# Performance work log

Hardware: AMD Instinct MI355X
Metric: run time of the kernel (lower is better)

## Reference

```python
import jax, jax.numpy as jnp
import numpy as np

B, DIMX, DIMY, DIMH = 256, 128, 128, 128
SMOOTH, CONVEX = 2.0, 1.0
MAX_IT, TOL = 500, 1e-3
sp = jax.nn.softplus


def setup_inputs() -> dict:
    key = jax.random.key(0)
    ks = jax.random.split(key, 32)
    def p(k, *shape):
        # xavier-ish small init for weights/biases
        return (jax.random.normal(k, shape, dtype=jnp.float32) * 0.05)
    return {
        'x': jax.random.normal(ks[0], (B, DIMX), dtype=jnp.float32),
        'y': jax.random.normal(ks[1], (B, DIMY), dtype=jnp.float32),
        # first block (Wuus[0], Wyus[0], Wys[0], Wus[0])
        'wuu0_w': p(ks[2], DIMH, DIMX), 'wuu0_b': p(ks[3], DIMH),
        'wyu0_w': p(ks[4], DIMY, DIMX), 'wyu0_b': p(ks[5], DIMY),
        'wy0': p(ks[6], DIMH, DIMY),
        'wu0_w': p(ks[7], DIMH, DIMX), 'wu0_b': p(ks[8], DIMH),
        # middle block (Wuus[1], Wzus[0], Wzs[0], Wyus[1], Wys[1], Wus[1])
        'wuu1_w': p(ks[9], DIMH, DIMH), 'wuu1_b': p(ks[10], DIMH),
        'wzu1_w': p(ks[11], DIMH, DIMH), 'wzu1_b': p(ks[12], DIMH),
        'wz1': p(ks[13], DIMH, DIMH),
        'wyu1_w': p(ks[14], DIMY, DIMH), 'wyu1_b': p(ks[15], DIMY),
        'wy1': p(ks[16], DIMH, DIMY),
        'wu1_w': p(ks[17], DIMH, DIMH), 'wu1_b': p(ks[18], DIMH),
        # last block (Wzus[-1], Wzs[-1], Wyus[-1], Wys[-1], Wus[-1])
        'wzu2_w': p(ks[19], 1, DIMH), 'wzu2_b': p(ks[20], 1),
        'wz2': p(ks[21], 1, DIMH),
        'wyu2_w': p(ks[22], DIMY, DIMH), 'wyu2_b': p(ks[23], DIMY),
        'wy2': p(ks[24], 1, DIMY),
        'wu2_w': p(ks[25], 1, DIMH), 'wu2_b': p(ks[26], 1),
    }


def reference(x, y, wuu0_w, wuu0_b, wyu0_w, wyu0_b, wy0, wu0_w, wu0_b,
              wuu1_w, wuu1_b, wzu1_w, wzu1_b, wz1, wyu1_w, wyu1_b, wy1, wu1_w, wu1_b,
              wzu2_w, wzu2_b, wz2, wyu2_w, wyu2_b, wy2, wu2_w, wu2_b):
    # ICNN scalar output summed over batch (per-sample outputs decouple in y)
    def icnn_sum(y_):
        u0 = sp(x @ wuu0_w.T + wuu0_b)                                   # [B,H]
        z = sp((y_ * (x @ wyu0_w.T + wyu0_b)) @ wy0.T + x @ wu0_w.T + wu0_b)
        u1 = sp(u0 @ wuu1_w.T + wuu1_b)
        zu = sp(u0 @ wzu1_w.T + wzu1_b)
        z = sp((z * zu) @ jnp.clip(wz1, 0.0, 1e10).T
               + (y_ * (u0 @ wyu1_w.T + wyu1_b)) @ wy1.T
               + u0 @ wu1_w.T + wu1_b)
        zu2 = sp(u1 @ wzu2_w.T + wzu2_b)                                 # [B,1]
        z = ((z * zu2) @ jnp.clip(wz2, 0.0, 1e10).T
             + (y_ * (u1 @ wyu2_w.T + wyu2_b)) @ wy2.T
             + u1 @ wu2_w.T + wu2_b)                                     # [B,1]
        out = z + (0.5 / SMOOTH) * jnp.sum(y_ * y_, axis=1, keepdims=True)
        return jnp.sum(out)

    grad_icnn = jax.grad(icnn_sum)
    step = 2.0 * SMOOTH

    def body(carry, i):
        y1, done = carry
        g = grad_icnn(y1)
        y1_new = y1 + (step / (i + 1.0)) * (y - g)
        conv = jnp.mean(jnp.linalg.norm(y - g, axis=1)) < TOL
        y1 = jnp.where(done, y1, y1_new)  # freeze after 'break'
        return (y1, done | conv), None

    y1_init = jnp.ones_like(y)
    (y1, _), _ = jax.lax.scan(body, (y1_init, jnp.asarray(False)),
                              jnp.arange(MAX_IT, dtype=jnp.float32))
    f_ast1 = y1 + CONVEX * y
    return jnp.mean(f_ast1, axis=1).reshape(-1, 1)
```

## Files before the change

### kernel.cpp

```cpp
#include <hip/hip_runtime.h>
#include <math.h>

#define NB 256
#define N 128
#define NTHREADS 512
#define MAX_IT 500
#define ALF0 0.41256f
#define ALF1 1.73581f
#define ALF2 0.53115f
#define ALF3 0.89502f
#define SLICE 40
#define SLOT(k) ((((k) >> 5) * SLICE) + ((k) & 31))
#define LDSVEC (3 * SLICE + 32)


template <int CTRL>
__device__ __forceinline__ float dpp_add(float p) {
    return p + __int_as_float(__builtin_amdgcn_update_dpp(
                   0, __float_as_int(p), CTRL, 0xF, 0xF, true));
}
__device__ __forceinline__ float quad_sum(float p) {
    p = dpp_add<0xB1>(p);
    p = dpp_add<0x4E>(p);
    return p;
}
__device__ __forceinline__ float row_sum16(float p) {
    p = quad_sum(p);
    p = dpp_add<0x124>(p);
    p = dpp_add<0x128>(p);
    return p;
}
__device__ __forceinline__ float wave_sum(float p) {
    p += __shfl_xor(p, 1);
    p += __shfl_xor(p, 2);
    p += __shfl_xor(p, 4);
    p += __shfl_xor(p, 8);
    p += __shfl_xor(p, 16);
    p += __shfl_xor(p, 32);
    return p;
}
__device__ __forceinline__ float softplus_f(float s) {
    float e = __expf(-fabsf(s));
    return fmaxf(s, 0.f) + __logf(1.f + e);
}
__device__ __forceinline__ float sigmoid_f(float s) {
    float e = __expf(-fabsf(s));
    float r = 1.f / (1.f + e);
    return s >= 0.f ? r : 1.f - r;
}

__device__ __forceinline__ float mv_row(const float* __restrict__ W,
                                        const float* __restrict__ V,
                                        int k, int h) {
    const float4* wr = (const float4*)(W + k * N + h * 32);
    const float4* vr = (const float4*)(V + h * SLICE);
    float q0 = 0.f, q1 = 0.f, q2 = 0.f, q3 = 0.f;
#pragma unroll
    for (int i = 0; i < 8; ++i) {
        float4 w = wr[i], v = vr[i];
        q0 = fmaf(w.x, v.x, q0); q1 = fmaf(w.y, v.y, q1);
        q2 = fmaf(w.z, v.z, q2); q3 = fmaf(w.w, v.w, q3);
    }
    return quad_sum((q0 + q1) + (q2 + q3));
}

__global__ __launch_bounds__(NTHREADS, 2)
void picnn_solve(const float* __restrict__ x, const float* __restrict__ y,
                 const float* __restrict__ wuu0_w, const float* __restrict__ wuu0_b,
                 const float* __restrict__ wyu0_w, const float* __restrict__ wyu0_b,
                 const float* __restrict__ wy0,
                 const float* __restrict__ wu0_w, const float* __restrict__ wu0_b,
                 const float* __restrict__ wuu1_w, const float* __restrict__ wuu1_b,
                 const float* __restrict__ wzu1_w, const float* __restrict__ wzu1_b,
                 const float* __restrict__ wz1,
                 const float* __restrict__ wyu1_w, const float* __restrict__ wyu1_b,
                 const float* __restrict__ wy1,
                 const float* __restrict__ wu1_w, const float* __restrict__ wu1_b,
                 const float* __restrict__ wzu2_w, const float* __restrict__ wzu2_b,
                 const float* __restrict__ wz2,
                 const float* __restrict__ wyu2_w, const float* __restrict__ wyu2_b,
                 const float* __restrict__ wy2,
                 float* __restrict__ out)
{
    const int b = blockIdx.x;
    const int t = threadIdx.x;
    const int k = t >> 2;
    const int h = t & 3;
    const int wave = t >> 6;
    const int lane = t & 63;

    __shared__ __align__(16) float xv[LDSVEC];
    __shared__ __align__(16) float u0v[LDSVEC];
    __shared__ __align__(16) float u1v[LDSVEC];
    __shared__ __align__(16) float a0s[LDSVEC];
    __shared__ __align__(16) float a1s[LDSVEC];
    __shared__ __align__(16) float y1s[LDSVEC];
    __shared__ __align__(16) float t1s[LDSVEC];
    __shared__ __align__(16) float d2s[LDSVEC];
    __shared__ __align__(16) float d1s[LDSVEC];
    __shared__ float rp[8];
    __shared__ __align__(16) float4 img1[8 * NTHREADS];
    __shared__ __align__(16) float4 img2[8 * NTHREADS];

    if (t < N) xv[SLOT(t)] = x[b * N + t];
    __syncthreads();

    float u0k = softplus_f(mv_row(wuu0_w, xv, k, h) + wuu0_b[k]);
    float a0k = mv_row(wyu0_w, xv, k, h) + wyu0_b[k];
    float c0  = mv_row(wu0_w,  xv, k, h) + wu0_b[k];
    if (h == 0) { u0v[SLOT(k)] = u0k; a0s[SLOT(k)] = a0k; }
    __syncthreads();

    float u1k = softplus_f(mv_row(wuu1_w, u0v, k, h) + wuu1_b[k]);
    float zu  = softplus_f(mv_row(wzu1_w, u0v, k, h) + wzu1_b[k]);
    float a1k = mv_row(wyu1_w, u0v, k, h) + wyu1_b[k];
    float c1  = mv_row(wu1_w,  u0v, k, h) + wu1_b[k];
    if (h == 0) { u1v[SLOT(k)] = u1k; a1s[SLOT(k)] = a1k; }
    __syncthreads();

    float a2 = mv_row(wyu2_w, u1v, k, h) + wyu2_b[k];
    float dp;
    {
        const float4* wr = (const float4*)(wzu2_w + h * 32);
        const float4* vr = (const float4*)(u1v + h * SLICE);
        float q0 = 0.f, q1 = 0.f, q2 = 0.f, q3 = 0.f;
#pragma unroll
        for (int i = 0; i < 8; ++i) {
            float4 w = wr[i], v = vr[i];
            q0 = fmaf(w.x, v.x, q0); q1 = fmaf(w.y, v.y, q1);
            q2 = fmaf(w.z, v.z, q2); q3 = fmaf(w.w, v.w, q3);
        }
        float zu2 = softplus_f(quad_sum((q0 + q1) + (q2 + q3)) + wzu2_b[0]);
        dp = zu2 * fmaxf(wz2[k], 0.f);
    }

    float4 wf0[8], wf1[8], wf2[8];
    float4 wb0[8];
    {
        const float4* r0 = (const float4*)(wy0 + k * N + h * 32);
        const float4* r1 = (const float4*)(wz1 + k * N + h * 32);
        const float4* r2 = (const float4*)(wy1 + k * N + h * 32);
        const float4* a0r = (const float4*)(a0s + h * SLICE);
        const float4* a1r = (const float4*)(a1s + h * SLICE);
#pragma unroll
        for (int i = 0; i < 8; ++i) {
            float4 a = r0[i], s0 = a0r[i];
            a.x *= s0.x; a.y *= s0.y; a.z *= s0.z; a.w *= s0.w;
            wf0[i] = a;
            float4 z = r1[i];
            z.x = fmaxf(z.x, 0.f); z.y = fmaxf(z.y, 0.f);
            z.z = fmaxf(z.z, 0.f); z.w = fmaxf(z.w, 0.f);
            wf1[i] = z;
            float4 c = r2[i], s1 = a1r[i];
            c.x *= s1.x; c.y *= s1.y; c.z *= s1.z; c.w *= s1.w;
            wf2[i] = c;
        }
#pragma unroll
        for (int i = 0; i < 8; ++i) {
            int r = h * 32 + 4 * i;
            wb0[i].x = wy0[(r + 0) * N + k] * a0k;
            wb0[i].y = wy0[(r + 1) * N + k] * a0k;
            wb0[i].z = wy0[(r + 2) * N + k] * a0k;
            wb0[i].w = wy0[(r + 3) * N + k] * a0k;
            float4 z1c, c1c;
            z1c.x = fmaxf(wz1[(r + 0) * N + k], 0.f);
            z1c.y = fmaxf(wz1[(r + 1) * N + k], 0.f);
            z1c.z = fmaxf(wz1[(r + 2) * N + k], 0.f);
            z1c.w = fmaxf(wz1[(r + 3) * N + k], 0.f);
            img1[i * NTHREADS + t] = z1c;
            c1c.x = wy1[(r + 0) * N + k] * a1k;
            c1c.y = wy1[(r + 1) * N + k] * a1k;
            c1c.z = wy1[(r + 2) * N + k] * a1k;
            c1c.w = wy1[(r + 3) * N + k] * a1k;
            img2[i * NTHREADS + t] = c1c;
        }
    }

    const float yk = y[b * N + k];
    const float ye2 = yk - a2 * wy2[k];
    float y1v = 2.f * ye2;
    if (h == 0) y1s[SLOT(k)] = y1v;
    __syncthreads();

    for (int it = 1; it <= MAX_IT; ++it) {
        const float4* yr = (const float4*)(y1s + h * SLICE);
        float4 vv[8];
#pragma unroll
        for (int i = 0; i < 8; ++i) vv[i] = yr[i];
        if (it > 1) {
            const float4* rpv = (const float4*)rp;
            float4 ua = rpv[0], ub = rpv[1];
            float4 u = ua + ub;
            float tot = (u.x + u.y) + (u.z + u.w);
            if (tot < 4e-6f) break;
        }
        float p0 = 0.f, p1 = 0.f, p2 = 0.f, p3 = 0.f;
        float q0 = 0.f, q1 = 0.f, q2 = 0.f, q3 = 0.f;
#pragma unroll
        for (int i = 0; i < 8; ++i) {
            float4 v = vv[i];
            p0 = fmaf(wf0[i].x, v.x, p0); p1 = fmaf(wf0[i].y, v.y, p1);
            p2 = fmaf(wf0[i].z, v.z, p2); p3 = fmaf(wf0[i].w, v.w, p3);
            q0 = fmaf(wf2[i].x, v.x, q0); q1 = fmaf(wf2[i].y, v.y, q1);
            q2 = fmaf(wf2[i].z, v.z, q2); q3 = fmaf(wf2[i].w, v.w, q3);
        }
        float s1  = quad_sum((p0 + p1) + (p2 + p3)) + c0;
        float s2a = quad_sum((q0 + q1) + (q2 + q3));
        float e1 = __expf(-fabsf(s1));
        float z1 = fmaxf(s1, 0.f) + __logf(1.f + e1);
        float rr1 = 1.f / (1.f + e1);
        float sig1 = (s1 >= 0.f) ? rr1 : 1.f - rr1;
        if (h == 0) t1s[SLOT(k)] = z1 * zu;
        __syncthreads();

        const float4* t1r = (const float4*)(t1s + h * SLICE);
        p0 = p1 = p2 = p3 = 0.f;
#pragma unroll
        for (int i = 0; i < 8; ++i) {
            float4 v1 = t1r[i];
            p0 = fmaf(wf1[i].x, v1.x, p0); p1 = fmaf(wf1[i].y, v1.y, p1);
            p2 = fmaf(wf1[i].z, v1.z, p2); p3 = fmaf(wf1[i].w, v1.w, p3);
        }
        float s2 = quad_sum((p0 + p1) + (p2 + p3)) + s2a + c1;
        float d2 = dp * sigmoid_f(s2);
        if (h == 0) d2s[SLOT(k)] = d2;
        __syncthreads();

        const float4* d2r = (const float4*)(d2s + h * SLICE);
        p0 = p1 = p2 = p3 = 0.f; q0 = q1 = q2 = q3 = 0.f;
#pragma unroll
        for (int i = 0; i < 8; ++i) {
            float4 d = d2r[i];
            float4 w1 = img1[i * NTHREADS + t];
            float4 w2 = img2[i * NTHREADS + t];
            p0 = fmaf(w1.x, d.x, p0); p1 = fmaf(w1.y, d.y, p1);
            p2 = fmaf(w1.z, d.z, p2); p3 = fmaf(w1.w, d.w, p3);
            q0 = fmaf(w2.x, d.x, q0); q1 = fmaf(w2.y, d.y, q1);
            q2 = fmaf(w2.z, d.z, q2); q3 = fmaf(w2.w, d.w, q3);
        }
        float qv  = quad_sum((p0 + p1) + (p2 + p3));
        float gcp = quad_sum((q0 + q1) + (q2 + q3));
        float d1 = qv * zu * sig1;
        if (h == 0) d1s[SLOT(k)] = d1;
        __syncthreads();

        const float4* d1r = (const float4*)(d1s + h * SLICE);
        p0 = p1 = p2 = p3 = 0.f;
#pragma unroll
        for (int i = 0; i < 8; ++i) {
            float4 d = d1r[i];
            p0 = fmaf(wb0[i].x, d.x, p0); p1 = fmaf(wb0[i].y, d.y, p1);
            p2 = fmaf(wb0[i].z, d.z, p2); p3 = fmaf(wb0[i].w, d.w, p3);
        }
        float gbp = quad_sum((p0 + p1) + (p2 + p3));
        float rres = ye2 - fmaf(0.5f, y1v, gcp + gbp);
        int ph = (it - 1) & 3;
        float alf = (ph == 0) ? ALF0 : (ph == 1) ? ALF1
                  : (ph == 2) ? ALF2 : ALF3;
        y1v = fmaf(alf, rres, y1v);
        if (h == 0) y1s[SLOT(k)] = y1v;
        float rs = row_sum16(rres * rres);
        rs += __shfl_xor(rs, 16);
        rs += __shfl_xor(rs, 32);
        if (lane == 0) rp[wave] = rs;
        __syncthreads();
    }

    __syncthreads();
    float v = wave_sum(y1v + yk);
    if (lane == 0) rp[wave] = v;
    __syncthreads();
    if (t == 0) {
        float s = ((rp[0] + rp[1]) + (rp[2] + rp[3]))
                + ((rp[4] + rp[5]) + (rp[6] + rp[7]));
        out[b] = s * (1.f / 512.f);
    }
}

extern "C" void kernel_launch(void* const* d_in, const int* in_sizes, int n_in,
                              void* d_out, int out_size, void* d_ws, size_t ws_size,
                              hipStream_t stream) {
    const float* x      = (const float*)d_in[0];
    const float* y      = (const float*)d_in[1];
    const float* wuu0_w = (const float*)d_in[2];
    const float* wuu0_b = (const float*)d_in[3];
    const float* wyu0_w = (const float*)d_in[4];
    const float* wyu0_b = (const float*)d_in[5];
    const float* wy0    = (const float*)d_in[6];
    const float* wu0_w  = (const float*)d_in[7];
    const float* wu0_b  = (const float*)d_in[8];
    const float* wuu1_w = (const float*)d_in[9];
    const float* wuu1_b = (const float*)d_in[10];
    const float* wzu1_w = (const float*)d_in[11];
    const float* wzu1_b = (const float*)d_in[12];
    const float* wz1    = (const float*)d_in[13];
    const float* wyu1_w = (const float*)d_in[14];
    const float* wyu1_b = (const float*)d_in[15];
    const float* wy1    = (const float*)d_in[16];
    const float* wu1_w  = (const float*)d_in[17];
    const float* wu1_b  = (const float*)d_in[18];
    const float* wzu2_w = (const float*)d_in[19];
    const float* wzu2_b = (const float*)d_in[20];
    const float* wz2    = (const float*)d_in[21];
    const float* wyu2_w = (const float*)d_in[22];
    const float* wyu2_b = (const float*)d_in[23];
    const float* wy2    = (const float*)d_in[24];
    float* out = (float*)d_out;

    picnn_solve<<<dim3(NB), dim3(NTHREADS), 0, stream>>>(
        x, y, wuu0_w, wuu0_b, wyu0_w, wyu0_b, wy0, wu0_w, wu0_b,
        wuu1_w, wuu1_b, wzu1_w, wzu1_b, wz1, wyu1_w, wyu1_b, wy1, wu1_w, wu1_b,
        wzu2_w, wzu2_b, wz2, wyu2_w, wyu2_b, wy2, out);
}
```

Baseline: 146.1 us.

## Keep transposed weight slices in registers instead of LDS images

The two transposed weight images (clamped wz1 and wy1 scaled by a1k) move out of shared memory and into per-thread register arrays, and the VGPR budget is raised to 256 with the occupancy hint dropped. The backward matvec then reads weights from registers, removing 128 KB of LDS traffic per iteration. The y1 vector loads are also moved after the convergence check. The cost is register pressure: 48 float4 of weights per thread at 512 threads limits occupancy to one block per CU and risks spills.

After: 154.6 us. 5.8% more time.

```diff
diff --git a/kernel.cpp b/kernel.cpp
--- a/kernel.cpp
+++ b/kernel.cpp
@@ -64,7 +64,8 @@
     return quad_sum((q0 + q1) + (q2 + q3));
 }
 
-__global__ __launch_bounds__(NTHREADS, 2)
+__global__ __launch_bounds__(NTHREADS)
+__attribute__((amdgpu_num_vgpr(256)))
 void picnn_solve(const float* __restrict__ x, const float* __restrict__ y,
                  const float* __restrict__ wuu0_w, const float* __restrict__ wuu0_b,
                  const float* __restrict__ wyu0_w, const float* __restrict__ wyu0_b,
@@ -99,8 +100,6 @@
     __shared__ __align__(16) float d2s[LDSVEC];
     __shared__ __align__(16) float d1s[LDSVEC];
     __shared__ float rp[8];
-    __shared__ __align__(16) float4 img1[8 * NTHREADS];
-    __shared__ __align__(16) float4 img2[8 * NTHREADS];
 
     if (t < N) xv[SLOT(t)] = x[b * N + t];
     __syncthreads();
@@ -134,8 +133,7 @@
         dp = zu2 * fmaxf(wz2[k], 0.f);
     }
 
-    float4 wf0[8], wf1[8], wf2[8];
-    float4 wb0[8];
+    float4 wf0[8], wf1[8], wf2[8], wb0[8], wb1[8], wb2[8];
     {
         const float4* r0 = (const float4*)(wy0 + k * N + h * 32);
         const float4* r1 = (const float4*)(wz1 + k * N + h * 32);
@@ -162,17 +160,14 @@
             wb0[i].y = wy0[(r + 1) * N + k] * a0k;
             wb0[i].z = wy0[(r + 2) * N + k] * a0k;
             wb0[i].w = wy0[(r + 3) * N + k] * a0k;
-            float4 z1c, c1c;
-            z1c.x = fmaxf(wz1[(r + 0) * N + k], 0.f);
-            z1c.y = fmaxf(wz1[(r + 1) * N + k], 0.f);
-            z1c.z = fmaxf(wz1[(r + 2) * N + k], 0.f);
-            z1c.w = fmaxf(wz1[(r + 3) * N + k], 0.f);
-            img1[i * NTHREADS + t] = z1c;
-            c1c.x = wy1[(r + 0) * N + k] * a1k;
-            c1c.y = wy1[(r + 1) * N + k] * a1k;
-            c1c.z = wy1[(r + 2) * N + k] * a1k;
-            c1c.w = wy1[(r + 3) * N + k] * a1k;
-            img2[i * NTHREADS + t] = c1c;
+            wb1[i].x = fmaxf(wz1[(r + 0) * N + k], 0.f);
+            wb1[i].y = fmaxf(wz1[(r + 1) * N + k], 0.f);
+            wb1[i].z = fmaxf(wz1[(r + 2) * N + k], 0.f);
+            wb1[i].w = fmaxf(wz1[(r + 3) * N + k], 0.f);
+            wb2[i].x = wy1[(r + 0) * N + k] * a1k;
+            wb2[i].y = wy1[(r + 1) * N + k] * a1k;
+            wb2[i].z = wy1[(r + 2) * N + k] * a1k;
+            wb2[i].w = wy1[(r + 3) * N + k] * a1k;
         }
     }
 
@@ -183,10 +178,6 @@
     __syncthreads();
 
     for (int it = 1; it <= MAX_IT; ++it) {
-        const float4* yr = (const float4*)(y1s + h * SLICE);
-        float4 vv[8];
-#pragma unroll
-        for (int i = 0; i < 8; ++i) vv[i] = yr[i];
         if (it > 1) {
             const float4* rpv = (const float4*)rp;
             float4 ua = rpv[0], ub = rpv[1];
@@ -194,11 +185,12 @@
             float tot = (u.x + u.y) + (u.z + u.w);
             if (tot < 4e-6f) break;
         }
+        const float4* yr = (const float4*)(y1s + h * SLICE);
         float p0 = 0.f, p1 = 0.f, p2 = 0.f, p3 = 0.f;
         float q0 = 0.f, q1 = 0.f, q2 = 0.f, q3 = 0.f;
 #pragma unroll
         for (int i = 0; i < 8; ++i) {
-            float4 v = vv[i];
+            float4 v = yr[i];
             p0 = fmaf(wf0[i].x, v.x, p0); p1 = fmaf(wf0[i].y, v.y, p1);
             p2 = fmaf(wf0[i].z, v.z, p2); p3 = fmaf(wf0[i].w, v.w, p3);
             q0 = fmaf(wf2[i].x, v.x, q0); q1 = fmaf(wf2[i].y, v.y, q1);
@@ -231,12 +223,10 @@
 #pragma unroll
         for (int i = 0; i < 8; ++i) {
             float4 d = d2r[i];
-            float4 w1 = img1[i * NTHREADS + t];
-            float4 w2 = img2[i * NTHREADS + t];
-            p0 = fmaf(w1.x, d.x, p0); p1 = fmaf(w1.y, d.y, p1);
-            p2 = fmaf(w1.z, d.z, p2); p3 = fmaf(w1.w, d.w, p3);
-            q0 = fmaf(w2.x, d.x, q0); q1 = fmaf(w2.y, d.y, q1);
-            q2 = fmaf(w2.z, d.z, q2); q3 = fmaf(w2.w, d.w, q3);
+            p0 = fmaf(wb1[i].x, d.x, p0); p1 = fmaf(wb1[i].y, d.y, p1);
+            p2 = fmaf(wb1[i].z, d.z, p2); p3 = fmaf(wb1[i].w, d.w, p3);
+            q0 = fmaf(wb2[i].x, d.x, q0); q1 = fmaf(wb2[i].y, d.y, q1);
+            q2 = fmaf(wb2[i].z, d.z, q2); q3 = fmaf(wb2[i].w, d.w, q3);
         }
         float qv  = quad_sum((p0 + p1) + (p2 + p3));
         float gcp = quad_sum((q0 + q1) + (q2 + q3));
```
